# Kernel optimization log

Hardware: AMD Instinct MI355X
Metric: run time of the kernel (lower is better)

The kernel has to match this reference:

```python
import jax, jax.numpy as jnp
import numpy as np

N_USERS = 200000
N_ITEMS = 200000
F_DIM = 128   # raw embedding_dim of u_feature / i_feature
E_DIM = 64    # embed_dim
N_NODES = 100000
K = 24        # threshold for is_user=True (max sampled neighbors)


def setup_inputs() -> dict:
    key = jax.random.key(0)
    ks = jax.random.split(key, 16)
    s = 0.05
    return {
        "nodes": jax.random.randint(ks[0], (N_NODES,), 0, N_USERS),
        "n_feature": jax.random.normal(ks[1], (N_NODES, E_DIM), jnp.float32),
        "neigh_idx": jax.random.randint(ks[2], (N_NODES, K), 0, N_ITEMS),
        "u_weight": jax.random.normal(ks[3], (N_USERS, F_DIM), jnp.float32) * s,
        "i_weight": jax.random.normal(ks[4], (N_ITEMS, F_DIM), jnp.float32) * s,
        "uW": jax.random.normal(ks[5], (F_DIM, E_DIM), jnp.float32) * s,
        "ub": jax.random.normal(ks[6], (E_DIM,), jnp.float32) * s,
        "iW": jax.random.normal(ks[7], (F_DIM, E_DIM), jnp.float32) * s,
        "ib": jax.random.normal(ks[8], (E_DIM,), jnp.float32) * s,
        "aW1": jax.random.normal(ks[9], (2 * E_DIM, E_DIM), jnp.float32) * s,
        "ab1": jax.random.normal(ks[10], (E_DIM,), jnp.float32) * s,
        "aW2": jax.random.normal(ks[11], (E_DIM, E_DIM), jnp.float32) * s,
        "ab2": jax.random.normal(ks[12], (E_DIM,), jnp.float32) * s,
        "aW3": jax.random.normal(ks[13], (E_DIM, 1), jnp.float32) * s,
        "ab3": jax.random.normal(ks[14], (1,), jnp.float32) * s,
    }


def reference(nodes, n_feature, neigh_idx, u_weight, i_weight,
              uW, ub, iW, ib, aW1, ab1, aW2, ab2, aW3, ab3):
    # u_layer applied to gathered user rows (L0Dense in eval mode ~ dense linear)
    nodes_fea = u_weight[nodes] @ uW + ub                       # [N, d]

    # Project the item table once, then gather neighbors (same math, less traffic
    # than gathering raw features per neighbor): i_layer(ifeature.weight[neighs])
    i_proj = i_weight @ iW + ib                                 # [n_items, d]
    neighs = i_proj[neigh_idx]                                  # [N, K, d]

    # query = mean(node_feature + n_feature[i], dim=0) over a [1,d] tensor == the vector itself
    q = nodes_fea + n_feature                                   # [N, d]

    # attention MLP over concat(neighbor, query) -> softmax over K neighbors
    x = jnp.concatenate(
        [neighs, jnp.broadcast_to(q[:, None, :], neighs.shape)], axis=-1)  # [N, K, 2d]
    h = jax.nn.relu(x @ aW1 + ab1)                              # [N, K, d]
    h = jax.nn.relu(h @ aW2 + ab2)                              # [N, K, d]
    scores = (h @ aW3 + ab3)[..., 0]                            # [N, K]
    att_w = jax.nn.softmax(scores, axis=-1)                     # [N, K]

    # attention-weighted aggregation: neighs_feature.T @ att_w per node
    emb = jnp.einsum('nk,nkd->nd', att_w, neighs)               # [N, d]

    # scatter into the full embed_matrix [num_embeddings, d]
    embed_matrix = jnp.zeros((u_weight.shape[0], nodes_fea.shape[1]),
                             nodes_fea.dtype).at[nodes].set(emb)
    return nodes_fea, embed_matrix
```

## Files before the change

kernel.cpp:

```cpp
#include <hip/hip_runtime.h>
#include <hip/hip_bf16.h>

#define N_NODES 100000
#define N_USERS 200000
#define N_ITEMS 200000
#define KNEI 24
#define E 64
#define F 128

typedef __attribute__((ext_vector_type(8))) short bf16x8;
typedef __attribute__((ext_vector_type(4))) float f32x4;


__device__ inline float bf2f(short s) {
    unsigned u = ((unsigned)(unsigned short)s) << 16;
    return __uint_as_float(u);
}
__device__ inline short f2bf(float f) {
    __hip_bfloat16 h = __float2bfloat16(f);
    return *reinterpret_cast<short*>(&h);
}
__device__ inline bf16x8 pack8(float4 a, float4 b) {
    bf16x8 r;
    r[0] = f2bf(a.x); r[1] = f2bf(a.y); r[2] = f2bf(a.z); r[3] = f2bf(a.w);
    r[4] = f2bf(b.x); r[5] = f2bf(b.y); r[6] = f2bf(b.z); r[7] = f2bf(b.w);
    return r;
}

__global__ __launch_bounds__(256) void k_fuse(const float* __restrict__ iW,
                                              const float* __restrict__ aW1,
                                              const float* __restrict__ ib,
                                              const float* __restrict__ ab1,
                                              const float* __restrict__ aW2,
                                              const float* __restrict__ ab2,
                                              const float* __restrict__ aW3,
                                              float* __restrict__ Wp,
                                              float* __restrict__ bp,
                                              bf16x8* __restrict__ B2img,
                                              float* __restrict__ bw) {
    int g = blockIdx.x * 256 + threadIdx.x;
    if (g < 8192) {
        int f = g >> 6, c = g & 63;
        float s = 0.f;
        for (int j = 0; j < 64; j++) s = fmaf(iW[f * 64 + j], aW1[j * 64 + c], s);
        Wp[g] = s;
        if (g < 64) {
            float b = ab1[g];
            for (int j = 0; j < 64; j++) b = fmaf(ib[j], aW1[j * 64 + g], b);
            bp[g] = b;
        }
    } else if (g < 8192 + 512) {
        int h = g - 8192;
        int f = h >> 6, l = h & 63;
        int s = f >> 2, u = f & 3;
        int lo = l & 15, hi = l >> 4;
        bf16x8 b;
        #pragma unroll
        for (int e = 0; e < 8; e++)
            b[e] = f2bf(aW2[(size_t)(32 * s + 8 * hi + e) * 64 + 16 * u + lo]);
        B2img[h] = b;
        if (f == 0) {
            #pragma unroll
            for (int uu = 0; uu < 4; uu++) {
                bw[l * 8 + uu]     = ab2[16 * uu + lo];
                bw[l * 8 + 4 + uu] = aW3[16 * uu + lo];
            }
        }
    }
}


__global__ __launch_bounds__(256, 2) void k_item(const float* __restrict__ iwt,
                                                 const float* __restrict__ iW,
                                                 const float* __restrict__ ib,
                                                 const float* __restrict__ Wp,
                                                 const float* __restrict__ bp,
                                                 __hip_bfloat16* __restrict__ iproj,
                                                 __hip_bfloat16* __restrict__ iatt) {
    const int wave = threadIdx.x >> 6, lane = threadIdx.x & 63;
    const int lo = lane & 15, hi = lane >> 4;

    bf16x8 B1[4][4], B2[4][4];
    #pragma unroll
    for (int s = 0; s < 4; s++) {
        #pragma unroll
        for (int u = 0; u < 4; u++) {
            bf16x8 b1, b2;
            #pragma unroll
            for (int e = 0; e < 8; e++) {
                int k = 32 * s + 8 * hi + e;
                b1[e] = f2bf(iW[k * 64 + 16 * u + lo]);
                b2[e] = f2bf(Wp[k * 64 + 16 * u + lo]);
            }
            B1[s][u] = b1; B2[s][u] = b2;
        }
    }
    float bi[4], ba[4];
    #pragma unroll
    for (int u = 0; u < 4; u++) { bi[u] = ib[16 * u + lo]; ba[u] = bp[16 * u + lo]; }

    const int wid = blockIdx.x * 4 + wave;
    for (int t = wid; t < N_ITEMS / 16; t += 512 * 4) {
        int r0 = t * 16;
        const float4* Ap = reinterpret_cast<const float4*>(iwt + (size_t)(r0 + lo) * F);
        bf16x8 A[4];
        #pragma unroll
        for (int s = 0; s < 4; s++)
            A[s] = pack8(Ap[8 * s + 2 * hi], Ap[8 * s + 2 * hi + 1]);
        f32x4 acc1[4], acc2[4];
        #pragma unroll
        for (int u = 0; u < 4; u++) {
            acc1[u] = (f32x4){0.f, 0.f, 0.f, 0.f};
            acc2[u] = (f32x4){0.f, 0.f, 0.f, 0.f};
        }
        #pragma unroll
        for (int s = 0; s < 4; s++) {
            #pragma unroll
            for (int u = 0; u < 4; u++) {
                acc1[u] = __builtin_amdgcn_mfma_f32_16x16x32_bf16(A[s], B1[s][u], acc1[u], 0, 0, 0);
                acc2[u] = __builtin_amdgcn_mfma_f32_16x16x32_bf16(A[s], B2[s][u], acc2[u], 0, 0, 0);
            }
        }
        #pragma unroll
        for (int u = 0; u < 4; u++) {
            #pragma unroll
            for (int reg = 0; reg < 4; reg++) {
                size_t off = (size_t)(r0 + 4 * hi + reg) * E + 16 * u + lo;
                iproj[off] = __float2bfloat16(acc1[u][reg] + bi[u]);
                iatt[off]  = __float2bfloat16(acc2[u][reg] + ba[u]);
            }
        }
    }
}

__global__ __launch_bounds__(256, 2) void k_node1(const int* __restrict__ nodes,
                                                  const float* __restrict__ uwt,
                                                  const float* __restrict__ uW,
                                                  const float* __restrict__ ub,
                                                  float* __restrict__ out_nf,
                                                  int* __restrict__ winner) {
    const int wave = threadIdx.x >> 6, lane = threadIdx.x & 63;
    const int lo = lane & 15, hi = lane >> 4;

    bf16x8 B[4][4];
    #pragma unroll
    for (int s = 0; s < 4; s++) {
        #pragma unroll
        for (int u = 0; u < 4; u++) {
            bf16x8 b;
            #pragma unroll
            for (int e = 0; e < 8; e++) {
                int k = 32 * s + 8 * hi + e;
                b[e] = f2bf(uW[k * 64 + 16 * u + lo]);
            }
            B[s][u] = b;
        }
    }
    float bu[4];
    #pragma unroll
    for (int u = 0; u < 4; u++) bu[u] = ub[16 * u + lo];

    const int wid = blockIdx.x * 4 + wave;
    for (int t = wid; t < N_NODES / 16; t += 256 * 4) {
        int r0 = t * 16;
        int n = r0 + lo;
        int un = nodes[n];
        if (hi == 0) atomicMax(&winner[un], n);
        const float4* Ap = reinterpret_cast<const float4*>(uwt + (size_t)un * F);
        bf16x8 A[4];
        #pragma unroll
        for (int s = 0; s < 4; s++)
            A[s] = pack8(Ap[8 * s + 2 * hi], Ap[8 * s + 2 * hi + 1]);
        f32x4 acc[4];
        #pragma unroll
        for (int u = 0; u < 4; u++) acc[u] = (f32x4){0.f, 0.f, 0.f, 0.f};
        #pragma unroll
        for (int s = 0; s < 4; s++) {
            #pragma unroll
            for (int u = 0; u < 4; u++)
                acc[u] = __builtin_amdgcn_mfma_f32_16x16x32_bf16(A[s], B[s][u], acc[u], 0, 0, 0);
        }
        #pragma unroll
        for (int u = 0; u < 4; u++) {
            #pragma unroll
            for (int reg = 0; reg < 4; reg++)
                out_nf[(size_t)(r0 + 4 * hi + reg) * E + 16 * u + lo] = acc[u][reg] + bu[u];
        }
    }
}

__global__ __launch_bounds__(256, 2) void k_node2(const float* __restrict__ out_nf,
                                                  const float* __restrict__ nfeat,
                                                  const float* __restrict__ aW1,
                                                  __hip_bfloat16* __restrict__ qatt) {
    const int wave = threadIdx.x >> 6, lane = threadIdx.x & 63;
    const int lo = lane & 15, hi = lane >> 4;

    bf16x8 B[2][4];
    #pragma unroll
    for (int s = 0; s < 2; s++) {
        #pragma unroll
        for (int u = 0; u < 4; u++) {
            bf16x8 b;
            #pragma unroll
            for (int e = 0; e < 8; e++) {
                int k = 32 * s + 8 * hi + e;
                b[e] = f2bf(aW1[(size_t)(E + k) * 64 + 16 * u + lo]);
            }
            B[s][u] = b;
        }
    }

    const int wid = blockIdx.x * 4 + wave;
    for (int t = wid; t < N_NODES / 16; t += 256 * 4) {
        int r0 = t * 16;
        const float4* Op = reinterpret_cast<const float4*>(out_nf + (size_t)(r0 + lo) * E);
        const float4* Np = reinterpret_cast<const float4*>(nfeat + (size_t)(r0 + lo) * E);
        bf16x8 A[2];
        #pragma unroll
        for (int s = 0; s < 2; s++) {
            float4 o0 = Op[8 * s + 2 * hi], o1 = Op[8 * s + 2 * hi + 1];
            float4 n0 = Np[8 * s + 2 * hi], n1 = Np[8 * s + 2 * hi + 1];
            float4 q0 = make_float4(o0.x + n0.x, o0.y + n0.y, o0.z + n0.z, o0.w + n0.w);
            float4 q1 = make_float4(o1.x + n1.x, o1.y + n1.y, o1.z + n1.z, o1.w + n1.w);
            A[s] = pack8(q0, q1);
        }
        f32x4 acc[4];
        #pragma unroll
        for (int u = 0; u < 4; u++) acc[u] = (f32x4){0.f, 0.f, 0.f, 0.f};
        #pragma unroll
        for (int s = 0; s < 2; s++) {
            #pragma unroll
            for (int u = 0; u < 4; u++)
                acc[u] = __builtin_amdgcn_mfma_f32_16x16x32_bf16(A[s], B[s][u], acc[u], 0, 0, 0);
        }
        #pragma unroll
        for (int u = 0; u < 4; u++) {
            #pragma unroll
            for (int reg = 0; reg < 4; reg++)
                qatt[(size_t)(r0 + 4 * hi + reg) * E + 16 * u + lo] =
                    __float2bfloat16(acc[u][reg]);
        }
    }
}

__global__ __launch_bounds__(256) void k_att(const int* __restrict__ nodes,
                                             const int* __restrict__ nidx,
                                             const __hip_bfloat16* __restrict__ iproj,
                                             const __hip_bfloat16* __restrict__ iatt,
                                             const __hip_bfloat16* __restrict__ qatt,
                                             const bf16x8* __restrict__ B2img,
                                             const float* __restrict__ bw,
                                             const int* __restrict__ winner,
                                             float* __restrict__ outE) {
    __shared__ float s_scores[4][192];
    __shared__ int2  s_iw[4][192];
    const int wave = threadIdx.x >> 6, lane = threadIdx.x & 63;
    const int lo = lane & 15, hi = lane >> 4;
    const int n0 = (blockIdx.x * 4 + wave) * 8;

    bf16x8 Bf[8];
    #pragma unroll
    for (int f = 0; f < 8; f++) Bf[f] = B2img[f * 64 + lane];
    f32x4 bb = *reinterpret_cast<const f32x4*>(bw + lane * 8);
    f32x4 wv = *reinterpret_cast<const f32x4*>(bw + lane * 8 + 4);

    int idxs[12], nls[12];
    #pragma unroll
    for (int t = 0; t < 12; t++) {
        int r = t * 16 + lo;
        int nl = r / 24;
        nls[t] = nl;
        idxs[t] = nidx[(size_t)(n0 + nl) * KNEI + (r - nl * 24)];
        s_iw[wave][r].x = idxs[t];
    }

    #pragma unroll
    for (int t = 0; t < 12; t++) {
        const bf16x8* iarow = reinterpret_cast<const bf16x8*>(iatt + (size_t)idxs[t] * E);
        const bf16x8* qrow  = reinterpret_cast<const bf16x8*>(qatt + (size_t)(n0 + nls[t]) * E);
        f32x4 acc[4];
        #pragma unroll
        for (int u = 0; u < 4; u++)
            acc[u] = (f32x4){bb[u], bb[u], bb[u], bb[u]};
        #pragma unroll
        for (int s = 0; s < 2; s++) {
            bf16x8 ia = iarow[4 * s + hi];
            bf16x8 qa = qrow[4 * s + hi];
            bf16x8 a;
            #pragma unroll
            for (int e = 0; e < 8; e++) {
                float v = bf2f(ia[e]) + bf2f(qa[e]);
                a[e] = f2bf(fmaxf(v, 0.f));
            }
            #pragma unroll
            for (int u = 0; u < 4; u++)
                acc[u] = __builtin_amdgcn_mfma_f32_16x16x32_bf16(a, Bf[s * 4 + u], acc[u], 0, 0, 0);
        }
        f32x4 sum;
        #pragma unroll
        for (int reg = 0; reg < 4; reg++) {
            float v = 0.f;
            #pragma unroll
            for (int u = 0; u < 4; u++)
                v = fmaf(fmaxf(acc[u][reg], 0.f), wv[u], v);
            sum[reg] = v;
        }
        #pragma unroll
        for (int m = 1; m < 16; m <<= 1) {
            #pragma unroll
            for (int reg = 0; reg < 4; reg++)
                sum[reg] += __shfl_xor(sum[reg], m);
        }
        if (lo == 0)
            *reinterpret_cast<f32x4*>(&s_scores[wave][t * 16 + hi * 4]) = sum;
    }
    __syncthreads();

    const int half = lane >> 5, j = lane & 31;
    for (int p = 0; p < 4; p++) {
        int nd = 2 * p + half;
        int n = n0 + nd;
        float sc = (j < KNEI) ? s_scores[wave][nd * KNEI + j] : -1e30f;
        float mx = sc;
        #pragma unroll
        for (int m = 1; m < 32; m <<= 1) mx = fmaxf(mx, __shfl_xor(mx, m));
        float e = (j < KNEI) ? __expf(sc - mx) : 0.f;
        float ss = e;
        #pragma unroll
        for (int m = 1; m < 32; m <<= 1) ss += __shfl_xor(ss, m);
        float w = e / ss;
        if (j < KNEI) s_iw[wave][nd * KNEI + j].y = __float_as_int(w);

        float emb0 = 0.f, emb1 = 0.f;
        const char* ipb = reinterpret_cast<const char*>(iproj);
        #pragma unroll
        for (int k = 0; k < KNEI; k++) {
            int2 iw = s_iw[wave][nd * KNEI + k];
            float wk = __int_as_float(iw.y);
            unsigned u = *reinterpret_cast<const unsigned*>(
                ipb + (size_t)iw.x * 128 + j * 4);
            emb0 = fmaf(wk, __uint_as_float(u << 16), emb0);
            emb1 = fmaf(wk, __uint_as_float(u & 0xFFFF0000u), emb1);
        }
        int un = nodes[n];
        if (winner[un] == n) {
            float2 st = make_float2(emb0, emb1);
            *reinterpret_cast<float2*>(outE + (size_t)un * E + 2 * j) = st;
        }
    }
}

extern "C" void kernel_launch(void* const* d_in, const int* in_sizes, int n_in,
                              void* d_out, int out_size, void* d_ws, size_t ws_size,
                              hipStream_t stream) {
    const int*   nodes = (const int*)d_in[0];
    const float* nfeat = (const float*)d_in[1];
    const int*   nidx  = (const int*)d_in[2];
    const float* uwt   = (const float*)d_in[3];
    const float* iwt   = (const float*)d_in[4];
    const float* uW    = (const float*)d_in[5];
    const float* ub    = (const float*)d_in[6];
    const float* iW    = (const float*)d_in[7];
    const float* ib    = (const float*)d_in[8];
    const float* aW1   = (const float*)d_in[9];
    const float* ab1   = (const float*)d_in[10];
    const float* aW2   = (const float*)d_in[11];
    const float* ab2   = (const float*)d_in[12];
    const float* aW3   = (const float*)d_in[13];

    float* out_nf  = (float*)d_out;
    float* out_emb = out_nf + (size_t)N_NODES * E;

    char* ws = (char*)d_ws;
    __hip_bfloat16* iproj = (__hip_bfloat16*)(ws);
    __hip_bfloat16* iatt  = (__hip_bfloat16*)(ws + 25600000);
    __hip_bfloat16* qatt  = (__hip_bfloat16*)(ws + 51200000);
    int*            winner = (int*)(ws + 64000000);
    float*          Wp     = (float*)(ws + 64800000);
    float*          bp     = (float*)(ws + 64832768);
    bf16x8*         B2img  = (bf16x8*)(ws + 64833024);
    float*          bwimg  = (float*)(ws + 64841216);

    hipMemsetAsync(winner, 0xFF, (size_t)N_USERS * sizeof(int), stream);
    hipMemsetAsync(out_emb, 0, (size_t)N_USERS * E * sizeof(float), stream);

    k_fuse<<<34, 256, 0, stream>>>(iW, aW1, ib, ab1, aW2, ab2, aW3,
                                   Wp, bp, B2img, bwimg);
    k_item<<<512, 256, 0, stream>>>(iwt, iW, ib, Wp, bp, iproj, iatt);
    k_node1<<<256, 256, 0, stream>>>(nodes, uwt, uW, ub, out_nf, winner);
    k_node2<<<256, 256, 0, stream>>>(out_nf, nfeat, aW1, qatt);
    k_att<<<N_NODES / 32, 256, 0, stream>>>(nodes, nidx, iproj, iatt, qatt,
                                            B2img, bwimg, winner, out_emb);
}
```

Baseline: 208.1 us.

## Fuse node kernels, transpose attention MFMA, and widen aggregation loads

Merges the two node kernels so the query projection reuses the freshly computed node features through LDS instead of re-reading them from global memory. In the attention kernel it swaps the MFMA operand order so each lane ends up with per-neighbor scores, which removes the 16-wide shuffle reduction and the __syncthreads. It also packs the add+ReLU+bf16 conversion with a byte-permute and widens the neighbor-aggregation gathers to 8 bytes per lane. Biases are folded into the accumulator initial values. This saves a launch and global traffic, at the cost of a more involved operand layout that must stay consistent with the rewritten bias/weight image.

```diff
diff --git a/kernel.cpp b/kernel.cpp
--- a/kernel.cpp
+++ b/kernel.cpp
@@ -25,6 +25,21 @@
     r[0] = f2bf(a.x); r[1] = f2bf(a.y); r[2] = f2bf(a.z); r[3] = f2bf(a.w);
     r[4] = f2bf(b.x); r[5] = f2bf(b.y); r[6] = f2bf(b.z); r[7] = f2bf(b.w);
     return r;
+}
+__device__ inline bf16x8 pack8v(f32x4 a, f32x4 b) {
+    bf16x8 r;
+    r[0] = f2bf(a[0]); r[1] = f2bf(a[1]); r[2] = f2bf(a[2]); r[3] = f2bf(a[3]);
+    r[4] = f2bf(b[0]); r[5] = f2bf(b[1]); r[6] = f2bf(b[2]); r[7] = f2bf(b[3]);
+    return r;
+}
+__device__ inline unsigned addmax_pack(unsigned ia, unsigned qa) {
+    float al = __uint_as_float(ia << 16);
+    float ah = __uint_as_float(ia & 0xFFFF0000u);
+    float bl = __uint_as_float(qa << 16);
+    float bh = __uint_as_float(qa & 0xFFFF0000u);
+    float sl = fmaxf(al + bl, 0.f);
+    float sh = fmaxf(ah + bh, 0.f);
+    return __builtin_amdgcn_perm(__float_as_uint(sh), __float_as_uint(sl), 0x07060302u);
 }
 
 __global__ __launch_bounds__(256) void k_fuse(const float* __restrict__ iW,
@@ -37,7 +52,7 @@
                                               float* __restrict__ Wp,
                                               float* __restrict__ bp,
                                               bf16x8* __restrict__ B2img,
-                                              float* __restrict__ bw) {
+                                              float* __restrict__ bwB) {
     int g = blockIdx.x * 256 + threadIdx.x;
     if (g < 8192) {
         int f = g >> 6, c = g & 63;
@@ -59,12 +74,17 @@
         for (int e = 0; e < 8; e++)
             b[e] = f2bf(aW2[(size_t)(32 * s + 8 * hi + e) * 64 + 16 * u + lo]);
         B2img[h] = b;
-        if (f == 0) {
-            #pragma unroll
-            for (int uu = 0; uu < 4; uu++) {
-                bw[l * 8 + uu]     = ab2[16 * uu + lo];
-                bw[l * 8 + 4 + uu] = aW3[16 * uu + lo];
-            }
+    } else if (g < 8192 + 512 + 2048) {
+        int h = g - 8704;
+        int l = h >> 5, m = h & 31;
+        int hi = l >> 4;
+        if (m < 16) {
+            int u = m >> 2, reg = m & 3;
+            bwB[l * 32 + m] = ab2[16 * u + 4 * hi + reg];
+        } else {
+            int m2 = m - 16;
+            int u = m2 >> 2, reg = m2 & 3;
+            bwB[l * 32 + m] = aW3[16 * u + 4 * hi + reg];
         }
     }
 }
@@ -110,8 +130,8 @@
         f32x4 acc1[4], acc2[4];
         #pragma unroll
         for (int u = 0; u < 4; u++) {
-            acc1[u] = (f32x4){0.f, 0.f, 0.f, 0.f};
-            acc2[u] = (f32x4){0.f, 0.f, 0.f, 0.f};
+            acc1[u] = (f32x4){bi[u], bi[u], bi[u], bi[u]};
+            acc2[u] = (f32x4){ba[u], ba[u], ba[u], ba[u]};
         }
         #pragma unroll
         for (int s = 0; s < 4; s++) {
@@ -126,23 +146,27 @@
             #pragma unroll
             for (int reg = 0; reg < 4; reg++) {
                 size_t off = (size_t)(r0 + 4 * hi + reg) * E + 16 * u + lo;
-                iproj[off] = __float2bfloat16(acc1[u][reg] + bi[u]);
-                iatt[off]  = __float2bfloat16(acc2[u][reg] + ba[u]);
-            }
-        }
-    }
-}
-
-__global__ __launch_bounds__(256, 2) void k_node1(const int* __restrict__ nodes,
-                                                  const float* __restrict__ uwt,
-                                                  const float* __restrict__ uW,
-                                                  const float* __restrict__ ub,
-                                                  float* __restrict__ out_nf,
-                                                  int* __restrict__ winner) {
+                iproj[off] = __float2bfloat16(acc1[u][reg]);
+                iatt[off]  = __float2bfloat16(acc2[u][reg]);
+            }
+        }
+    }
+}
+
+__global__ __launch_bounds__(256, 2) void k_node(const int* __restrict__ nodes,
+                                                 const float* __restrict__ nfeat,
+                                                 const float* __restrict__ uwt,
+                                                 const float* __restrict__ uW,
+                                                 const float* __restrict__ ub,
+                                                 const float* __restrict__ aW1,
+                                                 float* __restrict__ out_nf,
+                                                 __hip_bfloat16* __restrict__ qatt,
+                                                 int* __restrict__ winner) {
+    __shared__ __align__(16) float qlds[4][16][68];
     const int wave = threadIdx.x >> 6, lane = threadIdx.x & 63;
     const int lo = lane & 15, hi = lane >> 4;
 
-    bf16x8 B[4][4];
+    bf16x8 B1[4][4], B2[2][4];
     #pragma unroll
     for (int s = 0; s < 4; s++) {
         #pragma unroll
@@ -153,7 +177,20 @@
                 int k = 32 * s + 8 * hi + e;
                 b[e] = f2bf(uW[k * 64 + 16 * u + lo]);
             }
-            B[s][u] = b;
+            B1[s][u] = b;
+        }
+    }
+    #pragma unroll
+    for (int s = 0; s < 2; s++) {
+        #pragma unroll
+        for (int u = 0; u < 4; u++) {
+            bf16x8 b;
+            #pragma unroll
+            for (int e = 0; e < 8; e++) {
+                int k = 32 * s + 8 * hi + e;
+                b[e] = f2bf(aW1[(size_t)(E + k) * 64 + 16 * u + lo]);
+            }
+            B2[s][u] = b;
         }
     }
     float bu[4];
@@ -173,73 +210,48 @@
             A[s] = pack8(Ap[8 * s + 2 * hi], Ap[8 * s + 2 * hi + 1]);
         f32x4 acc[4];
         #pragma unroll
-        for (int u = 0; u < 4; u++) acc[u] = (f32x4){0.f, 0.f, 0.f, 0.f};
+        for (int u = 0; u < 4; u++) acc[u] = (f32x4){bu[u], bu[u], bu[u], bu[u]};
         #pragma unroll
         for (int s = 0; s < 4; s++) {
             #pragma unroll
             for (int u = 0; u < 4; u++)
-                acc[u] = __builtin_amdgcn_mfma_f32_16x16x32_bf16(A[s], B[s][u], acc[u], 0, 0, 0);
-        }
-        #pragma unroll
-        for (int u = 0; u < 4; u++) {
-            #pragma unroll
-            for (int reg = 0; reg < 4; reg++)
-                out_nf[(size_t)(r0 + 4 * hi + reg) * E + 16 * u + lo] = acc[u][reg] + bu[u];
-        }
-    }
-}
-
-__global__ __launch_bounds__(256, 2) void k_node2(const float* __restrict__ out_nf,
-                                                  const float* __restrict__ nfeat,
-                                                  const float* __restrict__ aW1,
-                                                  __hip_bfloat16* __restrict__ qatt) {
-    const int wave = threadIdx.x >> 6, lane = threadIdx.x & 63;
-    const int lo = lane & 15, hi = lane >> 4;
-
-    bf16x8 B[2][4];
-    #pragma unroll
-    for (int s = 0; s < 2; s++) {
-        #pragma unroll
-        for (int u = 0; u < 4; u++) {
-            bf16x8 b;
-            #pragma unroll
-            for (int e = 0; e < 8; e++) {
-                int k = 32 * s + 8 * hi + e;
-                b[e] = f2bf(aW1[(size_t)(E + k) * 64 + 16 * u + lo]);
-            }
-            B[s][u] = b;
-        }
-    }
-
-    const int wid = blockIdx.x * 4 + wave;
-    for (int t = wid; t < N_NODES / 16; t += 256 * 4) {
-        int r0 = t * 16;
-        const float4* Op = reinterpret_cast<const float4*>(out_nf + (size_t)(r0 + lo) * E);
+                acc[u] = __builtin_amdgcn_mfma_f32_16x16x32_bf16(A[s], B1[s][u], acc[u], 0, 0, 0);
+        }
+        #pragma unroll
+        for (int u = 0; u < 4; u++) {
+            #pragma unroll
+            for (int reg = 0; reg < 4; reg++) {
+                float v = acc[u][reg];
+                out_nf[(size_t)(r0 + 4 * hi + reg) * E + 16 * u + lo] = v;
+                qlds[wave][4 * hi + reg][16 * u + lo] = v;
+            }
+        }
         const float4* Np = reinterpret_cast<const float4*>(nfeat + (size_t)(r0 + lo) * E);
-        bf16x8 A[2];
+        bf16x8 A2[2];
         #pragma unroll
         for (int s = 0; s < 2; s++) {
-            float4 o0 = Op[8 * s + 2 * hi], o1 = Op[8 * s + 2 * hi + 1];
-            float4 n0 = Np[8 * s + 2 * hi], n1 = Np[8 * s + 2 * hi + 1];
-            float4 q0 = make_float4(o0.x + n0.x, o0.y + n0.y, o0.z + n0.z, o0.w + n0.w);
-            float4 q1 = make_float4(o1.x + n1.x, o1.y + n1.y, o1.z + n1.z, o1.w + n1.w);
-            A[s] = pack8(q0, q1);
-        }
-        f32x4 acc[4];
-        #pragma unroll
-        for (int u = 0; u < 4; u++) acc[u] = (f32x4){0.f, 0.f, 0.f, 0.f};
+            f32x4 qa = *reinterpret_cast<const f32x4*>(&qlds[wave][lo][32 * s + 8 * hi]);
+            f32x4 qb = *reinterpret_cast<const f32x4*>(&qlds[wave][lo][32 * s + 8 * hi + 4]);
+            float4 n0v = Np[8 * s + 2 * hi], n1v = Np[8 * s + 2 * hi + 1];
+            f32x4 fa = {qa[0] + n0v.x, qa[1] + n0v.y, qa[2] + n0v.z, qa[3] + n0v.w};
+            f32x4 fb = {qb[0] + n1v.x, qb[1] + n1v.y, qb[2] + n1v.z, qb[3] + n1v.w};
+            A2[s] = pack8v(fa, fb);
+        }
+        f32x4 acc2[4];
+        #pragma unroll
+        for (int u = 0; u < 4; u++) acc2[u] = (f32x4){0.f, 0.f, 0.f, 0.f};
         #pragma unroll
         for (int s = 0; s < 2; s++) {
             #pragma unroll
             for (int u = 0; u < 4; u++)
-                acc[u] = __builtin_amdgcn_mfma_f32_16x16x32_bf16(A[s], B[s][u], acc[u], 0, 0, 0);
+                acc2[u] = __builtin_amdgcn_mfma_f32_16x16x32_bf16(A2[s], B2[s][u], acc2[u], 0, 0, 0);
         }
         #pragma unroll
         for (int u = 0; u < 4; u++) {
             #pragma unroll
             for (int reg = 0; reg < 4; reg++)
                 qatt[(size_t)(r0 + 4 * hi + reg) * E + 16 * u + lo] =
-                    __float2bfloat16(acc[u][reg]);
+                    __float2bfloat16(acc2[u][reg]);
         }
     }
 }
@@ -250,7 +262,7 @@
                                              const __hip_bfloat16* __restrict__ iatt,
                                              const __hip_bfloat16* __restrict__ qatt,
                                              const bf16x8* __restrict__ B2img,
-                                             const float* __restrict__ bw,
+                                             const float* __restrict__ bwB,
                                              const int* __restrict__ winner,
                                              float* __restrict__ outE) {
     __shared__ float s_scores[4][192];
@@ -259,68 +271,66 @@
     const int lo = lane & 15, hi = lane >> 4;
     const int n0 = (blockIdx.x * 4 + wave) * 8;
 
-    bf16x8 Bf[8];
-    #pragma unroll
-    for (int f = 0; f < 8; f++) Bf[f] = B2img[f * 64 + lane];
-    f32x4 bb = *reinterpret_cast<const f32x4*>(bw + lane * 8);
-    f32x4 wv = *reinterpret_cast<const f32x4*>(bw + lane * 8 + 4);
-
-    int idxs[12], nls[12];
+    bf16x8 Af[8];
+    #pragma unroll
+    for (int f = 0; f < 8; f++) Af[f] = B2img[f * 64 + lane];
+    f32x4 bbv[4], wvv[4];
+    #pragma unroll
+    for (int u = 0; u < 4; u++) {
+        bbv[u] = *reinterpret_cast<const f32x4*>(bwB + lane * 32 + 4 * u);
+        wvv[u] = *reinterpret_cast<const f32x4*>(bwB + lane * 32 + 16 + 4 * u);
+    }
+
+    int idxs[12];
     #pragma unroll
     for (int t = 0; t < 12; t++) {
         int r = t * 16 + lo;
         int nl = r / 24;
-        nls[t] = nl;
         idxs[t] = nidx[(size_t)(n0 + nl) * KNEI + (r - nl * 24)];
         s_iw[wave][r].x = idxs[t];
     }
 
     #pragma unroll
     for (int t = 0; t < 12; t++) {
-        const bf16x8* iarow = reinterpret_cast<const bf16x8*>(iatt + (size_t)idxs[t] * E);
-        const bf16x8* qrow  = reinterpret_cast<const bf16x8*>(qatt + (size_t)(n0 + nls[t]) * E);
+        int r = t * 16 + lo;
+        int nl = r / 24;
+        const uint4* iarow = reinterpret_cast<const uint4*>(
+            reinterpret_cast<const char*>(iatt) + (size_t)idxs[t] * 128);
+        const uint4* qrow = reinterpret_cast<const uint4*>(
+            reinterpret_cast<const char*>(qatt) + (size_t)(n0 + nl) * 128);
         f32x4 acc[4];
         #pragma unroll
-        for (int u = 0; u < 4; u++)
-            acc[u] = (f32x4){bb[u], bb[u], bb[u], bb[u]};
+        for (int u = 0; u < 4; u++) acc[u] = bbv[u];
         #pragma unroll
         for (int s = 0; s < 2; s++) {
-            bf16x8 ia = iarow[4 * s + hi];
-            bf16x8 qa = qrow[4 * s + hi];
-            bf16x8 a;
-            #pragma unroll
-            for (int e = 0; e < 8; e++) {
-                float v = bf2f(ia[e]) + bf2f(qa[e]);
-                a[e] = f2bf(fmaxf(v, 0.f));
-            }
+            uint4 ia = iarow[4 * s + hi];
+            uint4 qa = qrow[4 * s + hi];
+            bf16x8 hfr;
+            unsigned* hp = reinterpret_cast<unsigned*>(&hfr);
+            hp[0] = addmax_pack(ia.x, qa.x);
+            hp[1] = addmax_pack(ia.y, qa.y);
+            hp[2] = addmax_pack(ia.z, qa.z);
+            hp[3] = addmax_pack(ia.w, qa.w);
             #pragma unroll
             for (int u = 0; u < 4; u++)
-                acc[u] = __builtin_amdgcn_mfma_f32_16x16x32_bf16(a, Bf[s * 4 + u], acc[u], 0, 0, 0);
-        }
-        f32x4 sum;
-        #pragma unroll
-        for (int reg = 0; reg < 4; reg++) {
-            float v = 0.f;
-            #pragma unroll
-            for (int u = 0; u < 4; u++)
-                v = fmaf(fmaxf(acc[u][reg], 0.f), wv[u], v);
-            sum[reg] = v;
-        }
-        #pragma unroll
-        for (int m = 1; m < 16; m <<= 1) {
+                acc[u] = __builtin_amdgcn_mfma_f32_16x16x32_bf16(Af[4 * s + u], hfr, acc[u], 0, 0, 0);
+        }
+        float part = 0.f;
+        #pragma unroll
+        for (int u = 0; u < 4; u++) {
             #pragma unroll
             for (int reg = 0; reg < 4; reg++)
-                sum[reg] += __shfl_xor(sum[reg], m);
-        }
-        if (lo == 0)
-            *reinterpret_cast<f32x4*>(&s_scores[wave][t * 16 + hi * 4]) = sum;
-    }
-    __syncthreads();
+                part = fmaf(fmaxf(acc[u][reg], 0.f), wvv[u][reg], part);
+        }
+        part += __shfl_xor(part, 16);
+        part += __shfl_xor(part, 32);
+        if (hi == 0) s_scores[wave][r] = part;
+    }
 
     const int half = lane >> 5, j = lane & 31;
+    #pragma unroll
     for (int p = 0; p < 4; p++) {
         int nd = 2 * p + half;
-        int n = n0 + nd;
         float sc = (j < KNEI) ? s_scores[wave][nd * KNEI + j] : -1e30f;
         float mx = sc;
         #pragma unroll
@@ -329,25 +339,29 @@
         float ss = e;
         #pragma unroll
         for (int m = 1; m < 32; m <<= 1) ss += __shfl_xor(ss, m);
-        float w = e / ss;
-        if (j < KNEI) s_iw[wave][nd * KNEI + j].y = __float_as_int(w);
-
-        float emb0 = 0.f, emb1 = 0.f;
-        const char* ipb = reinterpret_cast<const char*>(iproj);
+        if (j < KNEI) s_iw[wave][nd * KNEI + j].y = __float_as_int(e / ss);
+    }
+
+    const int qd = lane >> 4, jj = lane & 15;
+    const char* ipb = reinterpret_cast<const char*>(iproj);
+    #pragma unroll
+    for (int p = 0; p < 2; p++) {
+        int nd = 4 * p + qd;
+        int n = n0 + nd;
+        float4 emb = make_float4(0.f, 0.f, 0.f, 0.f);
         #pragma unroll
         for (int k = 0; k < KNEI; k++) {
             int2 iw = s_iw[wave][nd * KNEI + k];
             float wk = __int_as_float(iw.y);
-            unsigned u = *reinterpret_cast<const unsigned*>(
-                ipb + (size_t)iw.x * 128 + j * 4);
-            emb0 = fmaf(wk, __uint_as_float(u << 16), emb0);
-            emb1 = fmaf(wk, __uint_as_float(u & 0xFFFF0000u), emb1);
+            uint2 uv = *reinterpret_cast<const uint2*>(ipb + (size_t)iw.x * 128 + jj * 8);
+            emb.x = fmaf(wk, __uint_as_float(uv.x << 16), emb.x);
+            emb.y = fmaf(wk, __uint_as_float(uv.x & 0xFFFF0000u), emb.y);
+            emb.z = fmaf(wk, __uint_as_float(uv.y << 16), emb.z);
+            emb.w = fmaf(wk, __uint_as_float(uv.y & 0xFFFF0000u), emb.w);
         }
         int un = nodes[n];
-        if (winner[un] == n) {
-            float2 st = make_float2(emb0, emb1);
-            *reinterpret_cast<float2*>(outE + (size_t)un * E + 2 * j) = st;
-        }
+        if (winner[un] == n)
+            *reinterpret_cast<float4*>(outE + (size_t)un * E + 4 * jj) = emb;
     }
 }
 
@@ -380,16 +394,16 @@
     float*          Wp     = (float*)(ws + 64800000);
     float*          bp     = (float*)(ws + 64832768);
     bf16x8*         B2img  = (bf16x8*)(ws + 64833024);
-    float*          bwimg  = (float*)(ws + 64841216);
+    float*          bwB    = (float*)(ws + 64841216);
 
     hipMemsetAsync(winner, 0xFF, (size_t)N_USERS * sizeof(int), stream);
     hipMemsetAsync(out_emb, 0, (size_t)N_USERS * E * sizeof(float), stream);
 
-    k_fuse<<<34, 256, 0, stream>>>(iW, aW1, ib, ab1, aW2, ab2, aW3,
-                                   Wp, bp, B2img, bwimg);
+    k_fuse<<<42, 256, 0, stream>>>(iW, aW1, ib, ab1, aW2, ab2, aW3,
+                                   Wp, bp, B2img, bwB);
     k_item<<<512, 256, 0, stream>>>(iwt, iW, ib, Wp, bp, iproj, iatt);
-    k_node1<<<256, 256, 0, stream>>>(nodes, uwt, uW, ub, out_nf, winner);
-    k_node2<<<256, 256, 0, stream>>>(out_nf, nfeat, aW1, qatt);
+    k_node<<<256, 256, 0, stream>>>(nodes, nfeat, uwt, uW, ub, aW1,
+                                    out_nf, qatt, winner);
     k_att<<<N_NODES / 32, 256, 0, stream>>>(nodes, nidx, iproj, iatt, qatt,
-                                            B2img, bwimg, winner, out_emb);
-}
+                                            B2img, bwB, winner, out_emb);
+}
```

After: 226.4 us. 8.8% more time.

## Fold biases into MFMA init, pack bf16 add-relu, widen gather, drop barrier

Applied to the files above, without the earlier changes.

Biases are now folded into the MFMA accumulator initialisation instead of being added afterwards. The add+relu+bf16 pack in the attention kernel uses a byte-permute that truncates rather than rounds. The __syncthreads is removed, which looks safe because each wave only touches its own shared slices. The softmax is split into its own pass, and the aggregation now has each lane gather 8 bytes (4 features) per neighbor with float4 stores, halving the number of passes. The truncation changes rounding slightly.

```diff
diff --git a/kernel.cpp b/kernel.cpp
--- a/kernel.cpp
+++ b/kernel.cpp
@@ -25,6 +25,15 @@
     r[0] = f2bf(a.x); r[1] = f2bf(a.y); r[2] = f2bf(a.z); r[3] = f2bf(a.w);
     r[4] = f2bf(b.x); r[5] = f2bf(b.y); r[6] = f2bf(b.z); r[7] = f2bf(b.w);
     return r;
+}
+__device__ inline unsigned addmax_pack(unsigned ia, unsigned qa) {
+    float al = __uint_as_float(ia << 16);
+    float ah = __uint_as_float(ia & 0xFFFF0000u);
+    float bl = __uint_as_float(qa << 16);
+    float bh = __uint_as_float(qa & 0xFFFF0000u);
+    float sl = fmaxf(al + bl, 0.f);
+    float sh = fmaxf(ah + bh, 0.f);
+    return __builtin_amdgcn_perm(__float_as_uint(sh), __float_as_uint(sl), 0x07060302u);
 }
 
 __global__ __launch_bounds__(256) void k_fuse(const float* __restrict__ iW,
@@ -110,8 +119,8 @@
         f32x4 acc1[4], acc2[4];
         #pragma unroll
         for (int u = 0; u < 4; u++) {
-            acc1[u] = (f32x4){0.f, 0.f, 0.f, 0.f};
-            acc2[u] = (f32x4){0.f, 0.f, 0.f, 0.f};
+            acc1[u] = (f32x4){bi[u], bi[u], bi[u], bi[u]};
+            acc2[u] = (f32x4){ba[u], ba[u], ba[u], ba[u]};
         }
         #pragma unroll
         for (int s = 0; s < 4; s++) {
@@ -126,8 +135,8 @@
             #pragma unroll
             for (int reg = 0; reg < 4; reg++) {
                 size_t off = (size_t)(r0 + 4 * hi + reg) * E + 16 * u + lo;
-                iproj[off] = __float2bfloat16(acc1[u][reg] + bi[u]);
-                iatt[off]  = __float2bfloat16(acc2[u][reg] + ba[u]);
+                iproj[off] = __float2bfloat16(acc1[u][reg]);
+                iatt[off]  = __float2bfloat16(acc2[u][reg]);
             }
         }
     }
@@ -173,7 +182,7 @@
             A[s] = pack8(Ap[8 * s + 2 * hi], Ap[8 * s + 2 * hi + 1]);
         f32x4 acc[4];
         #pragma unroll
-        for (int u = 0; u < 4; u++) acc[u] = (f32x4){0.f, 0.f, 0.f, 0.f};
+        for (int u = 0; u < 4; u++) acc[u] = (f32x4){bu[u], bu[u], bu[u], bu[u]};
         #pragma unroll
         for (int s = 0; s < 4; s++) {
             #pragma unroll
@@ -184,7 +193,7 @@
         for (int u = 0; u < 4; u++) {
             #pragma unroll
             for (int reg = 0; reg < 4; reg++)
-                out_nf[(size_t)(r0 + 4 * hi + reg) * E + 16 * u + lo] = acc[u][reg] + bu[u];
+                out_nf[(size_t)(r0 + 4 * hi + reg) * E + 16 * u + lo] = acc[u][reg];
         }
     }
 }
@@ -277,25 +286,27 @@
 
     #pragma unroll
     for (int t = 0; t < 12; t++) {
-        const bf16x8* iarow = reinterpret_cast<const bf16x8*>(iatt + (size_t)idxs[t] * E);
-        const bf16x8* qrow  = reinterpret_cast<const bf16x8*>(qatt + (size_t)(n0 + nls[t]) * E);
+        const uint4* iarow = reinterpret_cast<const uint4*>(
+            reinterpret_cast<const char*>(iatt) + (size_t)idxs[t] * 128);
+        const uint4* qrow = reinterpret_cast<const uint4*>(
+            reinterpret_cast<const char*>(qatt) + (size_t)(n0 + nls[t]) * 128);
         f32x4 acc[4];
         #pragma unroll
         for (int u = 0; u < 4; u++)
             acc[u] = (f32x4){bb[u], bb[u], bb[u], bb[u]};
         #pragma unroll
         for (int s = 0; s < 2; s++) {
-            bf16x8 ia = iarow[4 * s + hi];
-            bf16x8 qa = qrow[4 * s + hi];
-            bf16x8 a;
-            #pragma unroll
-            for (int e = 0; e < 8; e++) {
-                float v = bf2f(ia[e]) + bf2f(qa[e]);
-                a[e] = f2bf(fmaxf(v, 0.f));
-            }
+            uint4 ia = iarow[4 * s + hi];
+            uint4 qa = qrow[4 * s + hi];
+            bf16x8 hfr;
+            unsigned* hp = reinterpret_cast<unsigned*>(&hfr);
+            hp[0] = addmax_pack(ia.x, qa.x);
+            hp[1] = addmax_pack(ia.y, qa.y);
+            hp[2] = addmax_pack(ia.z, qa.z);
+            hp[3] = addmax_pack(ia.w, qa.w);
             #pragma unroll
             for (int u = 0; u < 4; u++)
-                acc[u] = __builtin_amdgcn_mfma_f32_16x16x32_bf16(a, Bf[s * 4 + u], acc[u], 0, 0, 0);
+                acc[u] = __builtin_amdgcn_mfma_f32_16x16x32_bf16(hfr, Bf[s * 4 + u], acc[u], 0, 0, 0);
         }
         f32x4 sum;
         #pragma unroll
@@ -315,12 +326,11 @@
         if (lo == 0)
             *reinterpret_cast<f32x4*>(&s_scores[wave][t * 16 + hi * 4]) = sum;
     }
-    __syncthreads();
 
     const int half = lane >> 5, j = lane & 31;
+    #pragma unroll
     for (int p = 0; p < 4; p++) {
         int nd = 2 * p + half;
-        int n = n0 + nd;
         float sc = (j < KNEI) ? s_scores[wave][nd * KNEI + j] : -1e30f;
         float mx = sc;
         #pragma unroll
@@ -329,25 +339,29 @@
         float ss = e;
         #pragma unroll
         for (int m = 1; m < 32; m <<= 1) ss += __shfl_xor(ss, m);
-        float w = e / ss;
-        if (j < KNEI) s_iw[wave][nd * KNEI + j].y = __float_as_int(w);
-
-        float emb0 = 0.f, emb1 = 0.f;
-        const char* ipb = reinterpret_cast<const char*>(iproj);
+        if (j < KNEI) s_iw[wave][nd * KNEI + j].y = __float_as_int(e / ss);
+    }
+
+    const int qd = lane >> 4, jj = lane & 15;
+    const char* ipb = reinterpret_cast<const char*>(iproj);
+    #pragma unroll
+    for (int p = 0; p < 2; p++) {
+        int nd = 4 * p + qd;
+        int n = n0 + nd;
+        float4 emb = make_float4(0.f, 0.f, 0.f, 0.f);
         #pragma unroll
         for (int k = 0; k < KNEI; k++) {
             int2 iw = s_iw[wave][nd * KNEI + k];
             float wk = __int_as_float(iw.y);
-            unsigned u = *reinterpret_cast<const unsigned*>(
-                ipb + (size_t)iw.x * 128 + j * 4);
-            emb0 = fmaf(wk, __uint_as_float(u << 16), emb0);
-            emb1 = fmaf(wk, __uint_as_float(u & 0xFFFF0000u), emb1);
+            uint2 uv = *reinterpret_cast<const uint2*>(ipb + (size_t)iw.x * 128 + jj * 8);
+            emb.x = fmaf(wk, __uint_as_float(uv.x << 16), emb.x);
+            emb.y = fmaf(wk, __uint_as_float(uv.x & 0xFFFF0000u), emb.y);
+            emb.z = fmaf(wk, __uint_as_float(uv.y << 16), emb.z);
+            emb.w = fmaf(wk, __uint_as_float(uv.y & 0xFFFF0000u), emb.w);
         }
         int un = nodes[n];
-        if (winner[un] == n) {
-            float2 st = make_float2(emb0, emb1);
-            *reinterpret_cast<float2*>(outE + (size_t)un * E + 2 * j) = st;
-        }
+        if (winner[un] == n)
+            *reinterpret_cast<float4*>(outE + (size_t)un * E + 4 * jj) = emb;
     }
 }
 
```

Measured after the change: 228.6 us. +9.9%, slower.
